# Kernel optimization log

Hardware: AMD Instinct MI355X
Metric: run time of the kernel (lower is better)

## Reference

```python
import jax, jax.numpy as jnp
import numpy as np

B, LS, LL = 1024, 128, 2048
E, VOCAB = 16, 160000
NH, KD = 8, 6
LSH_DIM, TOPK = 16, 48
D_ITEM = 3 * E  # 48
EPS = 1e-3  # keras LayerNormalization default epsilon


def setup_inputs() -> dict:
    key = jax.random.key(0)
    ks = iter(jax.random.split(key, 64))
    def nk():
        return next(ks)
    def ids(shape):
        return jax.random.randint(nk(), shape, 0, VOCAB, dtype=jnp.int32)
    inp = {}
    for n in ['uid', 'utag1', 'utag2', 'utag3', 'utag4',
              'label_goods_ids', 'label_shop_ids', 'label_cate_ids']:
        inp[n] = ids((B,))
    for n in ['shortterm_goods_ids', 'shortterm_shop_ids', 'shortterm_cate_ids']:
        inp[n] = ids((B, LS))
    for n in ['longterm_goods_ids', 'longterm_shop_ids', 'longterm_cate_ids']:
        inp[n] = ids((B, LL))
    def rn(shape, s=0.05):
        return (jax.random.normal(nk(), shape) * s).astype(jnp.float32)
    inp['emb_table'] = rn((VOCAB, E))
    inp['H'] = rn((D_ITEM, LSH_DIM), 1.0)  # non-trainable random projection
    for p in ('s', 'l'):
        inp[p + 'Wq'] = rn((D_ITEM, NH, KD)); inp[p + 'bq'] = jnp.zeros((NH, KD), jnp.float32)
        inp[p + 'Wk'] = rn((D_ITEM, NH, KD)); inp[p + 'bk'] = jnp.zeros((NH, KD), jnp.float32)
        inp[p + 'Wv'] = rn((D_ITEM, NH, KD)); inp[p + 'bv'] = jnp.zeros((NH, KD), jnp.float32)
        inp[p + 'Wo'] = rn((NH, KD, D_ITEM)); inp[p + 'bo'] = jnp.zeros((D_ITEM,), jnp.float32)
    Din = D_ITEM + 5 * E + D_ITEM + D_ITEM  # 224
    inp['W1'] = rn((Din, 200)); inp['b1'] = jnp.zeros((200,), jnp.float32)
    inp['g1'] = jnp.ones((200,), jnp.float32); inp['be1'] = jnp.zeros((200,), jnp.float32)
    inp['W2'] = rn((200, 80)); inp['b2'] = jnp.zeros((80,), jnp.float32)
    inp['g2'] = jnp.ones((80,), jnp.float32); inp['be2'] = jnp.zeros((80,), jnp.float32)
    inp['W3'] = rn((80, 1)); inp['b3'] = jnp.zeros((1,), jnp.float32)
    return inp


def _ln(x, g, b):
    m = jnp.mean(x, axis=-1, keepdims=True)
    v = jnp.mean((x - m) ** 2, axis=-1, keepdims=True)
    return (x - m) * jax.lax.rsqrt(v + EPS) * g + b


def _mha(q, kv, mask3, Wq, bq, Wk, bk, Wv, bv, Wo, bo):
    # q: [B,1,D], kv: [B,K,D], mask3: [B,1,K] float (1=keep)
    qh = jnp.einsum('bqe,ehd->bqhd', q, Wq) + bq
    kh = jnp.einsum('bke,ehd->bkhd', kv, Wk) + bk
    vh = jnp.einsum('bke,ehd->bkhd', kv, Wv) + bv
    sc = jnp.einsum('bqhd,bkhd->bhqk', qh, kh) / jnp.sqrt(jnp.float32(KD))
    sc = sc + (1.0 - mask3[:, None, :, :]) * jnp.float32(-1e9)
    a = jax.nn.softmax(sc, axis=-1)
    o = jnp.einsum('bhqk,bkhd->bqhd', a, vh)
    return jnp.einsum('bqhd,hde->bqe', o, Wo) + bo


def reference(uid, utag1, utag2, utag3, utag4,
              label_goods_ids, label_shop_ids, label_cate_ids,
              shortterm_goods_ids, shortterm_shop_ids, shortterm_cate_ids,
              longterm_goods_ids, longterm_shop_ids, longterm_cate_ids,
              emb_table, H,
              sWq, sbq, sWk, sbk, sWv, sbv, sWo, sbo,
              lWq, lbq, lWk, lbk, lWv, lbv, lWo, lbo,
              W1, b1, g1, be1, W2, b2, g2, be2, W3, b3):
    short_mask = shortterm_goods_ids == 0  # padding_index == 0
    long_mask = longterm_goods_ids == 0

    def stack_embed(lst):
        X = jnp.stack([t if t.ndim == 2 else t[:, None] for t in lst], axis=2)  # [B,L,F]
        Xe = emb_table[X]  # [B,L,F,E]
        return Xe.reshape(Xe.shape[0], Xe.shape[1], -1)

    X_item = stack_embed([label_goods_ids, label_shop_ids, label_cate_ids])  # [B,1,48]
    X_user = stack_embed([uid, utag1, utag2, utag3, utag4])                  # [B,1,80]
    X_short = stack_embed([shortterm_goods_ids, shortterm_shop_ids, shortterm_cate_ids])  # [B,LS,48]
    X_long = stack_embed([longterm_goods_ids, longterm_shop_ids, longterm_cate_ids])      # [B,LL,48]

    # short-term interest
    slen = jnp.sum((~short_mask).astype(jnp.int32), axis=1)
    smask = (jnp.arange(LS)[None, :] < slen[:, None]).astype(jnp.float32)[:, None, :]
    short_int = _mha(X_item, X_short, smask, sWq, sbq, sWk, sbk, sWv, sbv, sWo, sbo)[:, 0]

    # long-term interest: LSH sign-hash hamming top-k retrieval
    series_codes = jnp.sign(jnp.einsum('ble,em->blm', X_long, H))  # [B,LL,16]
    item_codes = jnp.sign(jnp.einsum('ble,em->blm', X_item, H))    # [B,1,16]
    scores = jnp.sum((series_codes == item_codes).astype(jnp.float32), axis=-1)  # [B,LL]
    scores = jnp.where(long_mask, -jnp.inf, scores)
    _, idx = jax.lax.top_k(scores, TOPK)  # descending, padded entries last
    top_emb = jnp.take_along_axis(X_long, idx[:, :, None], axis=1)  # [B,TOPK,48]
    top_mask = jnp.take_along_axis(long_mask, idx, axis=1)
    llen = jnp.sum((~top_mask).astype(jnp.int32), axis=1)
    lmask = (jnp.arange(TOPK)[None, :] < llen[:, None]).astype(jnp.float32)[:, None, :]
    long_int = _mha(X_item, top_emb, lmask, lWq, lbq, lWk, lbk, lWv, lbv, lWo, lbo)[:, 0]

    x = jnp.concatenate([X_item[:, 0], X_user[:, 0], short_int, long_int], axis=1)  # [B,224]
    h1 = jax.nn.relu(_ln(x @ W1 + b1, g1, be1))
    h2 = jax.nn.relu(_ln(h1 @ W2 + b2, g2, be2))
    out = jax.nn.sigmoid(h2 @ W3 + b3)  # [B,1]
    return out
```

## Files before the change

kernel.cpp:

```cpp
#include <hip/hip_runtime.h>
#include <math.h>

#define BB 1024
#define LSx 128
#define LLx 2048
#define TOPKx 48

__global__ __launch_bounds__(256) void k_score_topk(
    const int* __restrict__ lg, const int* __restrict__ lsh, const int* __restrict__ lc,
    const int* __restrict__ ig, const int* __restrict__ ish, const int* __restrict__ ici,
    const float* __restrict__ emb, const float* __restrict__ Hm,
    int* __restrict__ sel)
{
  __shared__ float Xitem[48];
  __shared__ int icode[16];
  __shared__ signed char scores[LLx];
  __shared__ int hist[18];
  __shared__ int cnt_above;
  __shared__ int wsum[4];
  const int b = blockIdx.x, tid = threadIdx.x;

  if (tid < 48) {
    const int seg = tid >> 4, e = tid & 15;
    const int id = (seg == 0) ? ig[b] : (seg == 1) ? ish[b] : ici[b];
    Xitem[tid] = emb[(size_t)id * 16 + e];
  }
  if (tid < 18) hist[tid] = 0;
  if (tid == 0) cnt_above = 0;
  __syncthreads();
  if (tid < 16) {
    float dd = 0.f;
    for (int e = 0; e < 48; ++e) dd += Xitem[e] * Hm[e * 16 + tid];
    icode[tid] = (dd > 0.f) ? 1 : (dd < 0.f ? -1 : 0);
  }
  __syncthreads();

  for (int j = 0; j < LLx / 256; ++j) {
    const int l = j * 256 + tid;
    const size_t off = (size_t)b * LLx + l;
    const int gid = lg[off];
    int sc;
    if (gid == 0) {
      sc = -1;
    } else {
      const int sid = lsh[off], cid = lc[off];
      float d[16];
      #pragma unroll
      for (int m = 0; m < 16; ++m) d[m] = 0.f;
      const int ids3[3] = {gid, sid, cid};
      #pragma unroll
      for (int seg = 0; seg < 3; ++seg) {
        const float* row = emb + (size_t)ids3[seg] * 16;
        const float4 r0 = ((const float4*)row)[0];
        const float4 r1 = ((const float4*)row)[1];
        const float4 r2 = ((const float4*)row)[2];
        const float4 r3 = ((const float4*)row)[3];
        const float x[16] = {r0.x, r0.y, r0.z, r0.w, r1.x, r1.y, r1.z, r1.w,
                             r2.x, r2.y, r2.z, r2.w, r3.x, r3.y, r3.z, r3.w};
        const float* hb = Hm + seg * 256;
        #pragma unroll
        for (int i = 0; i < 16; ++i) {
          const float xi = x[i];
          #pragma unroll
          for (int mc = 0; mc < 4; ++mc) {
            const float4 h4 = *(const float4*)(hb + i * 16 + mc * 4);
            d[mc * 4 + 0] += xi * h4.x;
            d[mc * 4 + 1] += xi * h4.y;
            d[mc * 4 + 2] += xi * h4.z;
            d[mc * 4 + 3] += xi * h4.w;
          }
        }
      }
      sc = 0;
      #pragma unroll
      for (int m = 0; m < 16; ++m) {
        const int cs = (d[m] > 0.f) ? 1 : (d[m] < 0.f ? -1 : 0);
        sc += (cs == icode[m]) ? 1 : 0;
      }
    }
    scores[l] = (signed char)sc;
    atomicAdd(&hist[sc + 1], 1);
  }
  __syncthreads();

  int above = 0, tval = -1, need = 0;
  for (int s = 16; s >= -1; --s) {
    const int c = hist[s + 1];
    if (above + c >= TOPKx) { tval = s; need = TOPKx - above; break; }
    above += c;
  }

  const int base_l = tid * (LLx / 256);
  int cnt = 0;
  for (int j = 0; j < LLx / 256; ++j) cnt += (scores[base_l + j] == tval) ? 1 : 0;
  int v = cnt;
  const int lane = tid & 63, wave = tid >> 6;
  #pragma unroll
  for (int o = 1; o < 64; o <<= 1) {
    const int u = __shfl_up(v, o, 64);
    if (lane >= o) v += u;
  }
  if (lane == 63) wsum[wave] = v;
  __syncthreads();
  int rank = v - cnt;
  for (int w = 0; w < wave; ++w) rank += wsum[w];

  for (int j = 0; j < LLx / 256; ++j) {
    const int l = base_l + j;
    const int s = scores[l];
    if (s > tval) {
      const int slot = atomicAdd(&cnt_above, 1);
      sel[b * TOPKx + slot] = l;
    } else if (s == tval) {
      if (rank < need) sel[b * TOPKx + above + rank] = l;
      ++rank;
    }
  }
}

template<int K, int STRIDE, bool IS_LONG>
__global__ __launch_bounds__(128) void k_mha(
    const int* __restrict__ kg, const int* __restrict__ ks, const int* __restrict__ kc,
    const int* __restrict__ ig, const int* __restrict__ ish, const int* __restrict__ ici,
    const float* __restrict__ emb,
    const float* __restrict__ Wq, const float* __restrict__ bq,
    const float* __restrict__ Wk, const float* __restrict__ bk,
    const float* __restrict__ Wv, const float* __restrict__ bv,
    const float* __restrict__ Wo, const float* __restrict__ bo,
    const int* __restrict__ sel,
    float* __restrict__ outv)
{
  __shared__ float Xitem[48];
  __shared__ float qh[48];
  __shared__ __align__(16) float vhs[K][48];
  __shared__ float scs[8][K + 4];
  __shared__ float osm[48];
  __shared__ unsigned char validf[K];
  const int b = blockIdx.x, tid = threadIdx.x;

  if (tid < 48) {
    const int seg = tid >> 4, e = tid & 15;
    const int id = (seg == 0) ? ig[b] : (seg == 1) ? ish[b] : ici[b];
    Xitem[tid] = emb[(size_t)id * 16 + e];
  }
  __syncthreads();
  if (tid < 48) {
    float a = bq[tid];
    for (int e = 0; e < 48; ++e) a += Xitem[e] * Wq[e * 48 + tid];
    qh[tid] = a;
  }

  int gid = 0, sid = 0, cid = 0;
  if (tid < K) {
    const int pos = IS_LONG ? sel[b * TOPKx + tid] : tid;
    const size_t off = (size_t)b * STRIDE + pos;
    gid = kg[off]; sid = ks[off]; cid = kc[off];
  }
  const int nval = __syncthreads_count((tid < K) && (gid != 0));

  if (tid < K) {
    validf[tid] = IS_LONG ? (unsigned char)(gid != 0) : (unsigned char)(tid < nval);
    float kh[48], vh[48];
    #pragma unroll
    for (int j = 0; j < 48; ++j) { kh[j] = bk[j]; vh[j] = bv[j]; }
    const int ids3[3] = {gid, sid, cid};
    #pragma unroll
    for (int seg = 0; seg < 3; ++seg) {
      const float* row = emb + (size_t)ids3[seg] * 16;
      #pragma unroll
      for (int i4 = 0; i4 < 4; ++i4) {
        const float4 xv = ((const float4*)row)[i4];
        const float xs[4] = {xv.x, xv.y, xv.z, xv.w};
        #pragma unroll
        for (int c = 0; c < 4; ++c) {
          const int e = seg * 16 + i4 * 4 + c;
          const float* wkr = Wk + e * 48;
          const float* wvr = Wv + e * 48;
          const float xe = xs[c];
          #pragma unroll
          for (int j = 0; j < 48; ++j) {
            kh[j] += xe * wkr[j];
            vh[j] += xe * wvr[j];
          }
        }
      }
    }
    #pragma unroll
    for (int h = 0; h < 8; ++h) {
      float s = 0.f;
      #pragma unroll
      for (int d = 0; d < 6; ++d) s += qh[h * 6 + d] * kh[h * 6 + d];
      scs[h][tid] = s * 0.40824829046386301637f;
    }
    #pragma unroll
    for (int j = 0; j < 48; ++j) vhs[tid][j] = vh[j];
  }
  __syncthreads();

  {
    const int h = tid >> 4, l16 = tid & 15;
    float amax = -INFINITY;
    for (int k = l16; k < K; k += 16) if (validf[k]) amax = fmaxf(amax, scs[h][k]);
    #pragma unroll
    for (int m = 1; m < 16; m <<= 1) amax = fmaxf(amax, __shfl_xor(amax, m, 16));
    if (nval == 0) {
      for (int k = l16; k < K; k += 16) scs[h][k] = 1.0f / (float)K;
    } else {
      float ssum = 0.f;
      for (int k = l16; k < K; k += 16) {
        const float ev = validf[k] ? expf(scs[h][k] - amax) : 0.f;
        scs[h][k] = ev;
        ssum += ev;
      }
      #pragma unroll
      for (int m = 1; m < 16; m <<= 1) ssum += __shfl_xor(ssum, m, 16);
      const float inv = 1.0f / ssum;
      for (int k = l16; k < K; k += 16) scs[h][k] *= inv;
    }
  }
  __syncthreads();

  if (tid < 48) {
    const int h = tid / 6;
    float a = 0.f;
    for (int k = 0; k < K; ++k) a += scs[h][k] * vhs[k][tid];
    osm[tid] = a;
  }
  __syncthreads();
  if (tid < 48) {
    float r = bo[tid];
    for (int j = 0; j < 48; ++j) r += osm[j] * Wo[j * 48 + tid];
    outv[b * 48 + tid] = r;
  }
}

__device__ __forceinline__ float block_sum256(float v, float* red) {
  #pragma unroll
  for (int m = 32; m >= 1; m >>= 1) v += __shfl_xor(v, m, 64);
  const int lane = threadIdx.x & 63, wave = threadIdx.x >> 6;
  if (lane == 0) red[wave] = v;
  __syncthreads();
  const float t = red[0] + red[1] + red[2] + red[3];
  __syncthreads();
  return t;
}

__global__ __launch_bounds__(256) void k_mlp(
    const int* __restrict__ uid, const int* __restrict__ u1, const int* __restrict__ u2,
    const int* __restrict__ u3, const int* __restrict__ u4,
    const int* __restrict__ ig, const int* __restrict__ ish, const int* __restrict__ ici,
    const float* __restrict__ emb,
    const float* __restrict__ sint, const float* __restrict__ lint,
    const float* __restrict__ W1, const float* __restrict__ b1,
    const float* __restrict__ g1, const float* __restrict__ be1,
    const float* __restrict__ W2, const float* __restrict__ b2,
    const float* __restrict__ g2, const float* __restrict__ be2,
    const float* __restrict__ W3, const float* __restrict__ b3,
    float* __restrict__ out)
{
  __shared__ __align__(16) float x[224];
  __shared__ __align__(16) float h1[200];
  __shared__ float h2[80];
  __shared__ float red[4];
  const int b = blockIdx.x, tid = threadIdx.x;

  if (tid < 128) {
    const int e = tid & 15;
    int id;
    if (tid < 48) {
      const int seg = tid >> 4;
      id = (seg == 0) ? ig[b] : (seg == 1) ? ish[b] : ici[b];
    } else {
      const int f = (tid - 48) >> 4;
      id = (f == 0) ? uid[b] : (f == 1) ? u1[b] : (f == 2) ? u2[b] : (f == 3) ? u3[b] : u4[b];
    }
    x[tid] = emb[(size_t)id * 16 + e];
  } else if (tid < 176) {
    x[tid] = sint[b * 48 + (tid - 128)];
  } else if (tid < 224) {
    x[tid] = lint[b * 48 + (tid - 176)];
  }
  __syncthreads();

  float v = 0.f;
  if (tid < 200) {
    v = b1[tid];
    for (int i4 = 0; i4 < 56; ++i4) {
      const float4 xv = *(const float4*)(x + i4 * 4);
      const float* w = W1 + i4 * 4 * 200 + tid;
      v += xv.x * w[0];
      v += xv.y * w[200];
      v += xv.z * w[400];
      v += xv.w * w[600];
    }
  }
  const float mean1 = block_sum256((tid < 200) ? v : 0.f, red) * (1.0f / 200.0f);
  const float dv = (tid < 200) ? (v - mean1) : 0.f;
  const float var1 = block_sum256(dv * dv, red) * (1.0f / 200.0f);
  if (tid < 200) {
    const float y = (v - mean1) * rsqrtf(var1 + 1e-3f) * g1[tid] + be1[tid];
    h1[tid] = fmaxf(y, 0.f);
  }
  __syncthreads();

  float v2 = 0.f;
  if (tid < 80) {
    v2 = b2[tid];
    for (int i4 = 0; i4 < 50; ++i4) {
      const float4 xv = *(const float4*)(h1 + i4 * 4);
      const float* w = W2 + i4 * 4 * 80 + tid;
      v2 += xv.x * w[0];
      v2 += xv.y * w[80];
      v2 += xv.z * w[160];
      v2 += xv.w * w[240];
    }
  }
  const float mean2 = block_sum256((tid < 80) ? v2 : 0.f, red) * (1.0f / 80.0f);
  const float dv2 = (tid < 80) ? (v2 - mean2) : 0.f;
  const float var2 = block_sum256(dv2 * dv2, red) * (1.0f / 80.0f);
  if (tid < 80) {
    const float y = (v2 - mean2) * rsqrtf(var2 + 1e-3f) * g2[tid] + be2[tid];
    h2[tid] = fmaxf(y, 0.f);
  }
  __syncthreads();

  const float p = (tid < 80) ? h2[tid] * W3[tid] : 0.f;
  const float z = block_sum256(p, red);
  if (tid == 0) {
    out[b] = 1.0f / (1.0f + expf(-(z + b3[0])));
  }
}

extern "C" void kernel_launch(void* const* d_in, const int* in_sizes, int n_in,
                              void* d_out, int out_size, void* d_ws, size_t ws_size,
                              hipStream_t stream) {
  (void)in_sizes; (void)n_in; (void)out_size; (void)ws_size;
  const int* uid = (const int*)d_in[0];
  const int* u1  = (const int*)d_in[1];
  const int* u2  = (const int*)d_in[2];
  const int* u3  = (const int*)d_in[3];
  const int* u4  = (const int*)d_in[4];
  const int* ig  = (const int*)d_in[5];
  const int* ish = (const int*)d_in[6];
  const int* ici = (const int*)d_in[7];
  const int* sg  = (const int*)d_in[8];
  const int* ss  = (const int*)d_in[9];
  const int* scd = (const int*)d_in[10];
  const int* lg  = (const int*)d_in[11];
  const int* ls  = (const int*)d_in[12];
  const int* lcd = (const int*)d_in[13];
  const float* emb = (const float*)d_in[14];
  const float* Hm  = (const float*)d_in[15];
  const float* sWq = (const float*)d_in[16];
  const float* sbq = (const float*)d_in[17];
  const float* sWk = (const float*)d_in[18];
  const float* sbk = (const float*)d_in[19];
  const float* sWv = (const float*)d_in[20];
  const float* sbv = (const float*)d_in[21];
  const float* sWo = (const float*)d_in[22];
  const float* sbo = (const float*)d_in[23];
  const float* lWq = (const float*)d_in[24];
  const float* lbq = (const float*)d_in[25];
  const float* lWk = (const float*)d_in[26];
  const float* lbk = (const float*)d_in[27];
  const float* lWv = (const float*)d_in[28];
  const float* lbv = (const float*)d_in[29];
  const float* lWo = (const float*)d_in[30];
  const float* lbo = (const float*)d_in[31];
  const float* W1 = (const float*)d_in[32];
  const float* b1 = (const float*)d_in[33];
  const float* g1 = (const float*)d_in[34];
  const float* be1 = (const float*)d_in[35];
  const float* W2 = (const float*)d_in[36];
  const float* b2 = (const float*)d_in[37];
  const float* g2 = (const float*)d_in[38];
  const float* be2 = (const float*)d_in[39];
  const float* W3 = (const float*)d_in[40];
  const float* b3 = (const float*)d_in[41];
  float* out = (float*)d_out;

  int* sel = (int*)d_ws;
  float* sint = (float*)d_ws + BB * TOPKx;
  float* lint = sint + BB * 48;

  k_score_topk<<<dim3(BB), dim3(256), 0, stream>>>(lg, ls, lcd, ig, ish, ici, emb, Hm, sel);
  k_mha<128, 128, false><<<dim3(BB), dim3(128), 0, stream>>>(
      sg, ss, scd, ig, ish, ici, emb,
      sWq, sbq, sWk, sbk, sWv, sbv, sWo, sbo, (const int*)nullptr, sint);
  k_mha<48, 2048, true><<<dim3(BB), dim3(128), 0, stream>>>(
      lg, ls, lcd, ig, ish, ici, emb,
      lWq, lbq, lWk, lbk, lWv, lbv, lWo, lbo, sel, lint);
  k_mlp<<<dim3(BB), dim3(256), 0, stream>>>(
      uid, u1, u2, u3, u4, ig, ish, ici, emb,
      sint, lint, W1, b1, g1, be1, W2, b2, g2, be2, W3, b3, out);
}
```

Before: 331.7 us.

## Precompute per-vocab LSH projections and split K/V projection across thread halves

Adds a kernel that projects every embedding row through each 16x16 segment of H once for the whole vocabulary, so scoring sums three precomputed 16-float partials per position instead of doing 768 FMAs. The scoring kernel moves to 512 threads, each handling 4 positions with vectorized id loads and keeping scores in registers. The MHA kernels move to 256 threads, with one half computing K and the other V, which halves per-thread register accumulators. The trade is an extra pass writing about 30 MB of partials, which is more than the 6M gathered positions need, plus gathers from that larger table.

```diff
diff --git a/kernel.cpp b/kernel.cpp
--- a/kernel.cpp
+++ b/kernel.cpp
@@ -5,80 +5,81 @@
 #define LSx 128
 #define LLx 2048
 #define TOPKx 48
-
-__global__ __launch_bounds__(256) void k_score_topk(
+#define VOCABx 160000
+
+__global__ __launch_bounds__(256) void k_partial(
+    const float* __restrict__ emb, const float* __restrict__ Hm,
+    float* __restrict__ P)
+{
+  const int idx = blockIdx.x * 256 + threadIdx.x;
+  if (idx >= VOCABx * 48) return;
+  const int v = idx / 48;
+  const int r = idx - v * 48;
+  const int seg = r >> 4, m = r & 15;
+  const float* er = emb + (size_t)v * 16;
+  float a = 0.f;
+  #pragma unroll
+  for (int e = 0; e < 16; ++e) a += er[e] * Hm[(seg * 16 + e) * 16 + m];
+  P[idx] = a;
+}
+
+__global__ __launch_bounds__(512) void k_score_topk(
     const int* __restrict__ lg, const int* __restrict__ lsh, const int* __restrict__ lc,
     const int* __restrict__ ig, const int* __restrict__ ish, const int* __restrict__ ici,
-    const float* __restrict__ emb, const float* __restrict__ Hm,
+    const float* __restrict__ P,
     int* __restrict__ sel)
 {
-  __shared__ float Xitem[48];
-  __shared__ int icode[16];
   __shared__ signed char scores[LLx];
   __shared__ int hist[18];
+  __shared__ int icode[16];
   __shared__ int cnt_above;
-  __shared__ int wsum[4];
+  __shared__ int wsum[8];
   const int b = blockIdx.x, tid = threadIdx.x;
 
-  if (tid < 48) {
-    const int seg = tid >> 4, e = tid & 15;
-    const int id = (seg == 0) ? ig[b] : (seg == 1) ? ish[b] : ici[b];
-    Xitem[tid] = emb[(size_t)id * 16 + e];
-  }
   if (tid < 18) hist[tid] = 0;
   if (tid == 0) cnt_above = 0;
-  __syncthreads();
   if (tid < 16) {
-    float dd = 0.f;
-    for (int e = 0; e < 48; ++e) dd += Xitem[e] * Hm[e * 16 + tid];
-    icode[tid] = (dd > 0.f) ? 1 : (dd < 0.f ? -1 : 0);
-  }
-  __syncthreads();
-
-  for (int j = 0; j < LLx / 256; ++j) {
-    const int l = j * 256 + tid;
-    const size_t off = (size_t)b * LLx + l;
-    const int gid = lg[off];
+    const float d = P[(size_t)ig[b] * 48 + tid]
+                  + P[(size_t)ish[b] * 48 + 16 + tid]
+                  + P[(size_t)ici[b] * 48 + 32 + tid];
+    icode[tid] = (d > 0.f) ? 1 : (d < 0.f ? -1 : 0);
+  }
+  __syncthreads();
+
+  const int base_l = tid * 4;
+  const int4 g4 = ((const int4*)(lg + (size_t)b * LLx))[tid];
+  const int4 s4 = ((const int4*)(lsh + (size_t)b * LLx))[tid];
+  const int4 c4 = ((const int4*)(lc + (size_t)b * LLx))[tid];
+  const int gids[4] = {g4.x, g4.y, g4.z, g4.w};
+  const int sids[4] = {s4.x, s4.y, s4.z, s4.w};
+  const int cids[4] = {c4.x, c4.y, c4.z, c4.w};
+  int myscore[4];
+  #pragma unroll
+  for (int j = 0; j < 4; ++j) {
     int sc;
+    const int gid = gids[j];
     if (gid == 0) {
       sc = -1;
     } else {
-      const int sid = lsh[off], cid = lc[off];
-      float d[16];
-      #pragma unroll
-      for (int m = 0; m < 16; ++m) d[m] = 0.f;
-      const int ids3[3] = {gid, sid, cid};
-      #pragma unroll
-      for (int seg = 0; seg < 3; ++seg) {
-        const float* row = emb + (size_t)ids3[seg] * 16;
-        const float4 r0 = ((const float4*)row)[0];
-        const float4 r1 = ((const float4*)row)[1];
-        const float4 r2 = ((const float4*)row)[2];
-        const float4 r3 = ((const float4*)row)[3];
-        const float x[16] = {r0.x, r0.y, r0.z, r0.w, r1.x, r1.y, r1.z, r1.w,
-                             r2.x, r2.y, r2.z, r2.w, r3.x, r3.y, r3.z, r3.w};
-        const float* hb = Hm + seg * 256;
-        #pragma unroll
-        for (int i = 0; i < 16; ++i) {
-          const float xi = x[i];
-          #pragma unroll
-          for (int mc = 0; mc < 4; ++mc) {
-            const float4 h4 = *(const float4*)(hb + i * 16 + mc * 4);
-            d[mc * 4 + 0] += xi * h4.x;
-            d[mc * 4 + 1] += xi * h4.y;
-            d[mc * 4 + 2] += xi * h4.z;
-            d[mc * 4 + 3] += xi * h4.w;
-          }
-        }
-      }
+      const float4* pg = (const float4*)(P + (size_t)gid * 48);
+      const float4* ps = (const float4*)(P + (size_t)sids[j] * 48 + 16);
+      const float4* pc = (const float4*)(P + (size_t)cids[j] * 48 + 32);
       sc = 0;
       #pragma unroll
-      for (int m = 0; m < 16; ++m) {
-        const int cs = (d[m] > 0.f) ? 1 : (d[m] < 0.f ? -1 : 0);
-        sc += (cs == icode[m]) ? 1 : 0;
+      for (int q = 0; q < 4; ++q) {
+        const float4 a = pg[q], bb = ps[q], c = pc[q];
+        const float dx = a.x + bb.x + c.x;
+        const float dy = a.y + bb.y + c.y;
+        const float dz = a.z + bb.z + c.z;
+        const float dw = a.w + bb.w + c.w;
+        sc += ((dx > 0.f ? 1 : (dx < 0.f ? -1 : 0)) == icode[q * 4 + 0]);
+        sc += ((dy > 0.f ? 1 : (dy < 0.f ? -1 : 0)) == icode[q * 4 + 1]);
+        sc += ((dz > 0.f ? 1 : (dz < 0.f ? -1 : 0)) == icode[q * 4 + 2]);
+        sc += ((dw > 0.f ? 1 : (dw < 0.f ? -1 : 0)) == icode[q * 4 + 3]);
       }
     }
-    scores[l] = (signed char)sc;
+    myscore[j] = sc;
+    scores[base_l + j] = (signed char)sc;
     atomicAdd(&hist[sc + 1], 1);
   }
   __syncthreads();
@@ -90,9 +91,9 @@
     above += c;
   }
 
-  const int base_l = tid * (LLx / 256);
   int cnt = 0;
-  for (int j = 0; j < LLx / 256; ++j) cnt += (scores[base_l + j] == tval) ? 1 : 0;
+  #pragma unroll
+  for (int j = 0; j < 4; ++j) cnt += (myscore[j] == tval) ? 1 : 0;
   int v = cnt;
   const int lane = tid & 63, wave = tid >> 6;
   #pragma unroll
@@ -105,9 +106,10 @@
   int rank = v - cnt;
   for (int w = 0; w < wave; ++w) rank += wsum[w];
 
-  for (int j = 0; j < LLx / 256; ++j) {
+  #pragma unroll
+  for (int j = 0; j < 4; ++j) {
     const int l = base_l + j;
-    const int s = scores[l];
+    const int s = myscore[j];
     if (s > tval) {
       const int slot = atomicAdd(&cnt_above, 1);
       sel[b * TOPKx + slot] = l;
@@ -119,7 +121,7 @@
 }
 
 template<int K, int STRIDE, bool IS_LONG>
-__global__ __launch_bounds__(128) void k_mha(
+__global__ __launch_bounds__(256) void k_mha(
     const int* __restrict__ kg, const int* __restrict__ ks, const int* __restrict__ kc,
     const int* __restrict__ ig, const int* __restrict__ ish, const int* __restrict__ ici,
     const float* __restrict__ emb,
@@ -137,6 +139,8 @@
   __shared__ float osm[48];
   __shared__ unsigned char validf[K];
   const int b = blockIdx.x, tid = threadIdx.x;
+  const int role = tid >> 7;
+  const int p = tid & 127;
 
   if (tid < 48) {
     const int seg = tid >> 4, e = tid & 15;
@@ -151,18 +155,19 @@
   }
 
   int gid = 0, sid = 0, cid = 0;
-  if (tid < K) {
-    const int pos = IS_LONG ? sel[b * TOPKx + tid] : tid;
+  if (p < K) {
+    const int pos = IS_LONG ? sel[b * TOPKx + p] : p;
     const size_t off = (size_t)b * STRIDE + pos;
     gid = kg[off]; sid = ks[off]; cid = kc[off];
   }
-  const int nval = __syncthreads_count((tid < K) && (gid != 0));
-
-  if (tid < K) {
-    validf[tid] = IS_LONG ? (unsigned char)(gid != 0) : (unsigned char)(tid < nval);
-    float kh[48], vh[48];
+  const int nval = __syncthreads_count(role == 0 && p < K && gid != 0);
+
+  if (p < K) {
+    float acc[48];
+    const float* Wm = (role == 0) ? Wk : Wv;
+    const float* bm = (role == 0) ? bk : bv;
     #pragma unroll
-    for (int j = 0; j < 48; ++j) { kh[j] = bk[j]; vh[j] = bv[j]; }
+    for (int j = 0; j < 48; ++j) acc[j] = bm[j];
     const int ids3[3] = {gid, sid, cid};
     #pragma unroll
     for (int seg = 0; seg < 3; ++seg) {
@@ -174,30 +179,30 @@
         #pragma unroll
         for (int c = 0; c < 4; ++c) {
           const int e = seg * 16 + i4 * 4 + c;
-          const float* wkr = Wk + e * 48;
-          const float* wvr = Wv + e * 48;
+          const float* wr = Wm + e * 48;
           const float xe = xs[c];
           #pragma unroll
-          for (int j = 0; j < 48; ++j) {
-            kh[j] += xe * wkr[j];
-            vh[j] += xe * wvr[j];
-          }
+          for (int j = 0; j < 48; ++j) acc[j] += xe * wr[j];
         }
       }
     }
-    #pragma unroll
-    for (int h = 0; h < 8; ++h) {
-      float s = 0.f;
+    if (role == 0) {
+      validf[p] = IS_LONG ? (unsigned char)(gid != 0) : (unsigned char)(p < nval);
       #pragma unroll
-      for (int d = 0; d < 6; ++d) s += qh[h * 6 + d] * kh[h * 6 + d];
-      scs[h][tid] = s * 0.40824829046386301637f;
-    }
-    #pragma unroll
-    for (int j = 0; j < 48; ++j) vhs[tid][j] = vh[j];
-  }
-  __syncthreads();
-
-  {
+      for (int h = 0; h < 8; ++h) {
+        float s = 0.f;
+        #pragma unroll
+        for (int d = 0; d < 6; ++d) s += qh[h * 6 + d] * acc[h * 6 + d];
+        scs[h][p] = s * 0.40824829046386301637f;
+      }
+    } else {
+      #pragma unroll
+      for (int j = 0; j < 48; ++j) vhs[p][j] = acc[j];
+    }
+  }
+  __syncthreads();
+
+  if (tid < 128) {
     const int h = tid >> 4, l16 = tid & 15;
     float amax = -INFINITY;
     for (int k = l16; k < K; k += 16) if (validf[k]) amax = fmaxf(amax, scs[h][k]);
@@ -382,12 +387,14 @@
   int* sel = (int*)d_ws;
   float* sint = (float*)d_ws + BB * TOPKx;
   float* lint = sint + BB * 48;
-
-  k_score_topk<<<dim3(BB), dim3(256), 0, stream>>>(lg, ls, lcd, ig, ish, ici, emb, Hm, sel);
-  k_mha<128, 128, false><<<dim3(BB), dim3(128), 0, stream>>>(
+  float* P = lint + BB * 48;
+
+  k_partial<<<dim3((VOCABx * 48 + 255) / 256), dim3(256), 0, stream>>>(emb, Hm, P);
+  k_score_topk<<<dim3(BB), dim3(512), 0, stream>>>(lg, ls, lcd, ig, ish, ici, P, sel);
+  k_mha<128, 128, false><<<dim3(BB), dim3(256), 0, stream>>>(
       sg, ss, scd, ig, ish, ici, emb,
       sWq, sbq, sWk, sbk, sWv, sbv, sWo, sbo, (const int*)nullptr, sint);
-  k_mha<48, 2048, true><<<dim3(BB), dim3(128), 0, stream>>>(
+  k_mha<48, 2048, true><<<dim3(BB), dim3(256), 0, stream>>>(
       lg, ls, lcd, ig, ish, ici, emb,
       lWq, lbq, lWk, lbk, lWv, lbv, lWo, lbo, sel, lint);
   k_mlp<<<dim3(BB), dim3(256), 0, stream>>>(
```

After: 424.0 us. +27.8%, slower.
